# Kernel tuning notes

Measured on AMD Instinct MI355X. Metric: run time of the kernel, lower is better.

Reference implementation:

```python
import jax, jax.numpy as jnp
import numpy as np

B, T, D, H = 2, 2048, 1024, 16
HD = D // H  # head_dim = 64

def setup_inputs() -> dict:
    key = jax.random.key(0)
    ks = jax.random.split(key, 5)
    s = 0.02
    return {
        "x": jax.random.normal(ks[0], (B, T, D), dtype=jnp.float32),
        "w_qkv": jax.random.normal(ks[1], (3 * D, D), dtype=jnp.float32) * s,
        "b_qkv": jax.random.normal(ks[2], (3 * D,), dtype=jnp.float32) * s,
        "w_proj": jax.random.normal(ks[3], (D, D), dtype=jnp.float32) * s,
        "b_proj": jax.random.normal(ks[4], (D,), dtype=jnp.float32) * s,
    }

def reference(x, w_qkv, b_qkv, w_proj, b_proj):
    b, t, c = x.shape
    h, hd = H, HD
    scale = hd ** -0.5
    # qkv projection (torch Linear: x @ W^T + b)
    qkv = x @ w_qkv.T + b_qkv                      # [b, t, 3c]
    q, k, v = jnp.split(qkv, 3, axis=-1)
    # b t (h d) -> b h t d
    reshape = lambda z: z.reshape(b, t, h, hd).transpose(0, 2, 1, 3)
    q, k, v = reshape(q), reshape(k), reshape(v)
    scores = jnp.einsum("bhqd,bhkd->bhqk", q, k) * scale  # [b, h, t, t]
    causal = jnp.triu(jnp.ones((t, t), dtype=bool), k=1)   # True above diag
    scores = jnp.where(causal[None, None], -jnp.inf, scores)
    attn = jax.nn.softmax(scores, axis=-1)
    out = jnp.einsum("bhqk,bhkd->bhqd", attn, v)            # [b, h, t, d]
    out = out.transpose(0, 2, 1, 3).reshape(b, t, c)        # b h t d -> b t (h d)
    return out @ w_proj.T + b_proj
```

## Files before the change

### kernel.cpp

```cpp
#include <hip/hip_runtime.h>
#include <hip/hip_bf16.h>

#define Bq 2
#define Tq 2048
#define Dq 1024
#define Hq 16
#define HDq 64

typedef __attribute__((ext_vector_type(8))) short short8;
typedef __attribute__((ext_vector_type(4))) float f32x4;

__device__ __forceinline__ unsigned short f2bf(float f) {
  union { float f; unsigned int i; } v; v.f = f;
  unsigned int r = v.i + 0x7fffu + ((v.i >> 16) & 1u);
  return (unsigned short)(r >> 16);
}

__device__ __forceinline__ short8 cvt8(const float* __restrict__ g) {
  const float4* gp = (const float4*)g;
  float4 x0 = gp[0], x1 = gp[1];
  short8 v;
  v[0] = (short)f2bf(x0.x); v[1] = (short)f2bf(x0.y);
  v[2] = (short)f2bf(x0.z); v[3] = (short)f2bf(x0.w);
  v[4] = (short)f2bf(x1.x); v[5] = (short)f2bf(x1.y);
  v[6] = (short)f2bf(x1.z); v[7] = (short)f2bf(x1.w);
  return v;
}

__device__ __forceinline__ void async_cp16(const void* g, void* l) {
  __builtin_amdgcn_global_load_lds(
      (const __attribute__((address_space(1))) void*)g,
      (__attribute__((address_space(3))) void*)l, 16, 0, 0);
}

__device__ __forceinline__ void permswap(unsigned &a, unsigned &b) {
  asm("v_permlane32_swap_b32 %0, %1" : "+v"(a), "+v"(b));
  asm("v_permlane16_swap_b32 %0, %1" : "+v"(a), "+v"(b));
}

constexpr int NXC = (Bq * Tq * Dq) / 8;
constexpr int NW1C = (3 * Dq * Dq) / 8;
constexpr int NW2C = (Dq * Dq) / 8;

#define QSCL 0.18033688011112042f

__global__ __launch_bounds__(256)
void cvt_all(const float* __restrict__ x, const float* __restrict__ w1,
             const float* __restrict__ w2, unsigned short* __restrict__ xo,
             unsigned short* __restrict__ w1o, unsigned short* __restrict__ w2o)
{
  int i = blockIdx.x * 256 + threadIdx.x;
  const float* src; unsigned short* dst; int j;
  if (i < NXC)              { src = x;  dst = xo;  j = i; }
  else if (i < NXC + NW1C)  { src = w1; dst = w1o; j = i - NXC; }
  else                      { src = w2; dst = w2o; j = i - NXC - NW1C; }
  *(short8*)&dst[(size_t)j * 8] = cvt8(src + (size_t)j * 8);
}

template<int EPI, int BM_, int BN_>
__global__ __launch_bounds__(256)
void gemm_bt(const unsigned short* __restrict__ Ab, const unsigned short* __restrict__ Wb,
             const float* __restrict__ bias, float* __restrict__ outp,
             int K, int N,
             unsigned short* __restrict__ qo, unsigned short* __restrict__ ko,
             unsigned short* __restrict__ vo)
{
  constexpr int WM = BM_ / 2, WN = BN_ / 2;
  constexpr int NI = WM / 16;
  constexpr int NJ = WN / 16;
  constexpr int NAI = BM_ / 32;
  constexpr int NBI = BN_ / 32;
  __shared__ unsigned short As[2 * BM_ * 32];
  __shared__ unsigned short Bs[2 * BN_ * 32];

  const int t = threadIdx.x;
  const int lane = t & 63, w = t >> 6;
  const int m0 = blockIdx.y * BM_, n0 = blockIdx.x * BN_;
  const int fr = lane & 15, qd = lane >> 4;
  const int wm = (w >> 1) * WM, wn = (w & 1) * WN;

  f32x4 acc[NI][NJ] = {};

  for (int k0 = 0; k0 < K; k0 += 64) {
    __syncthreads();
    #pragma unroll
    for (int j = 0; j < NAI; j++) {
      int G = j * 256 + t;
      int panel = G / (BM_ * 4), rowg = (G / 4) % BM_, colg = G & 3;
      async_cp16(Ab + (size_t)(m0 + rowg) * K + k0 + panel * 32 + colg * 8, &As[G * 8]);
    }
    #pragma unroll
    for (int j = 0; j < NBI; j++) {
      int G = j * 256 + t;
      int panel = G / (BN_ * 4), rowg = (G / 4) % BN_, colg = G & 3;
      async_cp16(Wb + (size_t)(n0 + rowg) * K + k0 + panel * 32 + colg * 8, &Bs[G * 8]);
    }
    __syncthreads();
    #pragma unroll
    for (int kh = 0; kh < 2; kh++) {
      short8 af[NI], bf[NJ];
      #pragma unroll
      for (int ib = 0; ib < NI; ib++)
        af[ib] = *(const short8*)&As[kh * (BM_ * 32) + (wm + ib * 16 + fr) * 32 + qd * 8];
      #pragma unroll
      for (int jb = 0; jb < NJ; jb++)
        bf[jb] = *(const short8*)&Bs[kh * (BN_ * 32) + (wn + jb * 16 + fr) * 32 + qd * 8];
      #pragma unroll
      for (int ib = 0; ib < NI; ib++)
        #pragma unroll
        for (int jb = 0; jb < NJ; jb++)
          acc[ib][jb] = __builtin_amdgcn_mfma_f32_16x16x32_bf16(af[ib], bf[jb], acc[ib][jb], 0, 0, 0);
    }
  }

  #pragma unroll
  for (int jb = 0; jb < NJ; jb++) {
    int col = n0 + wn + jb * 16 + fr;
    float bv = bias[col];
    if (EPI == 0) {
      int which = col >> 10;
      int rem = col & 1023;
      int hh = rem >> 6, dd = rem & 63;
      #pragma unroll
      for (int ib = 0; ib < NI; ib++) {
        int row4 = m0 + wm + ib * 16 + qd * 4;
        int bb = row4 >> 11, tt = row4 & (Tq - 1);
        if (which == 2) {
          unsigned lo = (unsigned)f2bf(acc[ib][jb][0] + bv)
                      | ((unsigned)f2bf(acc[ib][jb][1] + bv) << 16);
          unsigned hi = (unsigned)f2bf(acc[ib][jb][2] + bv)
                      | ((unsigned)f2bf(acc[ib][jb][3] + bv) << 16);
          uint2 pk; pk.x = lo; pk.y = hi;
          *(uint2*)&vo[((size_t)(bb * Hq + hh) * HDq + dd) * Tq + tt] = pk;
        } else {
          unsigned short* dst = (which == 0) ? qo : ko;
          float scl = (which == 0) ? QSCL : 1.0f;
          #pragma unroll
          for (int r = 0; r < 4; r++)
            dst[((size_t)(bb * Hq + hh) * Tq + tt + r) * HDq + dd] =
                f2bf((acc[ib][jb][r] + bv) * scl);
        }
      }
    } else {
      #pragma unroll
      for (int ib = 0; ib < NI; ib++)
        #pragma unroll
        for (int r = 0; r < 4; r++) {
          int row = m0 + wm + ib * 16 + qd * 4 + r;
          outp[(size_t)row * N + col] = acc[ib][jb][r] + bv;
        }
    }
  }
}


template<bool DIAG>
__device__ __forceinline__ void strip_iter(
    const unsigned short* __restrict__ Ksb, const unsigned short* __restrict__ Vtsb,
    const short8 (&aq)[2], const short8 ones,
    int fr, int qd, int off0, int off1, int thr,
    f32x4 (&oacc)[4], f32x4& lacc)
{
  short8 bk[4][2];
  #pragma unroll
  for (int nb = 0; nb < 4; nb++) {
    bk[nb][0] = *(const short8*)&Ksb[(nb * 16 + fr) * 64 + off0];
    bk[nb][1] = *(const short8*)&Ksb[(nb * 16 + fr) * 64 + off1];
  }
  f32x4 s4[4] = {};
  __builtin_amdgcn_s_setprio(1);
  #pragma unroll
  for (int nb = 0; nb < 4; nb++)
    s4[nb] = __builtin_amdgcn_mfma_f32_16x16x32_bf16(bk[nb][0], aq[0], s4[nb], 0, 0, 0);
  #pragma unroll
  for (int nb = 0; nb < 4; nb++)
    s4[nb] = __builtin_amdgcn_mfma_f32_16x16x32_bf16(bk[nb][1], aq[1], s4[nb], 0, 0, 0);
  __builtin_amdgcn_s_setprio(0);

  unsigned x[4][2];
  #pragma unroll
  for (int nb = 0; nb < 4; nb++) {
    float p[4];
    #pragma unroll
    for (int reg = 0; reg < 4; reg++) {
      p[reg] = exp2f(s4[nb][reg]);
      if (DIAG && (nb * 16 + qd * 4 + reg) > thr) p[reg] = 0.f;
    }
    asm("v_cvt_pk_bf16_f32 %0, %1, %2" : "=v"(x[nb][0]) : "v"(p[0]), "v"(p[1]));
    asm("v_cvt_pk_bf16_f32 %0, %1, %2" : "=v"(x[nb][1]) : "v"(p[2]), "v"(p[3]));
  }
  permswap(x[0][0], x[1][0]);
  permswap(x[0][1], x[1][1]);
  permswap(x[2][0], x[3][0]);
  permswap(x[2][1], x[3][1]);

  short8 ap0, ap1;
  {
    union { unsigned u[4]; short8 s; } c0, c1;
    c0.u[0] = x[0][0]; c0.u[1] = x[0][1]; c0.u[2] = x[1][0]; c0.u[3] = x[1][1];
    c1.u[0] = x[2][0]; c1.u[1] = x[2][1]; c1.u[2] = x[3][0]; c1.u[3] = x[3][1];
    ap0 = c0.s; ap1 = c1.s;
  }

  short8 bv[4][2];
  #pragma unroll
  for (int db = 0; db < 4; db++) {
    bv[db][0] = *(const short8*)&Vtsb[(db * 16 + fr) * 64 + off0];
    bv[db][1] = *(const short8*)&Vtsb[(db * 16 + fr) * 64 + off1];
  }
  __builtin_amdgcn_s_setprio(1);
  lacc = __builtin_amdgcn_mfma_f32_16x16x32_bf16(ap0, ones, lacc, 0, 0, 0);
  lacc = __builtin_amdgcn_mfma_f32_16x16x32_bf16(ap1, ones, lacc, 0, 0, 0);
  #pragma unroll
  for (int db = 0; db < 4; db++) {
    oacc[db] = __builtin_amdgcn_mfma_f32_16x16x32_bf16(ap0, bv[db][0], oacc[db], 0, 0, 0);
    oacc[db] = __builtin_amdgcn_mfma_f32_16x16x32_bf16(ap1, bv[db][1], oacc[db], 0, 0, 0);
  }
  __builtin_amdgcn_s_setprio(0);
}

__global__ __launch_bounds__(256, 4)
void attn_fwd(const unsigned short* __restrict__ qb, const unsigned short* __restrict__ kb,
              const unsigned short* __restrict__ vtb, unsigned short* __restrict__ ab)
{
  __shared__ unsigned short Ks[2][64 * 64];
  __shared__ unsigned short Vts[2][64 * 64];

  const int t = threadIdx.x, w = t >> 6, lane = t & 63;
  const int fr = lane & 15, qd = lane >> 4;

  const int L  = (int)blockIdx.x;
  const int c  = L & 7;
  const int i  = L >> 3;
  const int q4 = i >> 5, j = i & 31;
  const int bh = c + 8 * q4;
  const int s  = (q4 & 1) ? j : 31 - j;
  const int s0 = s * 64;
  const int thr = w * 16 + fr;

  short8 aq[2];
  const unsigned short* Qg = qb + ((size_t)bh * Tq + s0) * HDq;
  #pragma unroll
  for (int cc = 0; cc < 2; cc++)
    aq[cc] = *(const short8*)(Qg + (w * 16 + fr) * 64 + cc * 32 + qd * 8);

  const unsigned short* Kbh = kb + (size_t)bh * Tq * HDq;
  const unsigned short* Vbh = vtb + (size_t)bh * HDq * Tq;

  const int off0 = ((qd ^ (fr & 7)) * 8);
  const int off1 = off0 ^ 32;

  const int G0 = 2 * w * 64 + lane, G1 = G0 + 64;
  const int r0 = G0 >> 3, g0 = (G0 & 7) ^ (r0 & 7);
  const int r1 = G1 >> 3, g1 = (G1 & 7) ^ (r1 & 7);

  short8 ones;
  #pragma unroll
  for (int jj = 0; jj < 8; jj++) ones[jj] = (short)0x3F80;

  f32x4 oacc[4] = {};
  f32x4 lacc = {};

  async_cp16(Kbh + (size_t)r0 * 64 + g0 * 8, &Ks[0][G0 * 8]);
  async_cp16(Vbh + (size_t)r0 * Tq + g0 * 8, &Vts[0][G0 * 8]);
  async_cp16(Kbh + (size_t)r1 * 64 + g1 * 8, &Ks[0][G1 * 8]);
  async_cp16(Vbh + (size_t)r1 * Tq + g1 * 8, &Vts[0][G1 * 8]);

  for (int kt = 0; kt < s; kt++) {
    const int cur = kt & 1, nxt = cur ^ 1;
    __syncthreads();
    const size_t kofs = (size_t)(kt + 1) * 64;
    async_cp16(Kbh + (kofs + r0) * 64 + g0 * 8, &Ks[nxt][G0 * 8]);
    async_cp16(Vbh + (size_t)r0 * Tq + kofs + g0 * 8, &Vts[nxt][G0 * 8]);
    async_cp16(Kbh + (kofs + r1) * 64 + g1 * 8, &Ks[nxt][G1 * 8]);
    async_cp16(Vbh + (size_t)r1 * Tq + kofs + g1 * 8, &Vts[nxt][G1 * 8]);
    strip_iter<false>(Ks[cur], Vts[cur], aq, ones, fr, qd, off0, off1, thr, oacc, lacc);
  }
  __syncthreads();
  strip_iter<true>(Ks[s & 1], Vts[s & 1], aq, ones, fr, qd, off0, off1, thr, oacc, lacc);

  #pragma unroll
  for (int reg = 0; reg < 4; reg++) {
    float linv = 1.0f / lacc[reg];
    size_t rowoff = ((size_t)(bh >> 4) * Tq + s0 + w * 16 + qd * 4 + reg) * Dq
                  + (bh & 15) * HDq;
    #pragma unroll
    for (int db = 0; db < 4; db++)
      ab[rowoff + db * 16 + fr] = f2bf(oacc[db][reg] * linv);
  }
}

extern "C" void kernel_launch(void* const* d_in, const int* in_sizes, int n_in,
                              void* d_out, int out_size, void* d_ws, size_t ws_size,
                              hipStream_t stream) {
  const float* x      = (const float*)d_in[0];
  const float* w_qkv  = (const float*)d_in[1];
  const float* b_qkv  = (const float*)d_in[2];
  const float* w_proj = (const float*)d_in[3];
  const float* b_proj = (const float*)d_in[4];
  float* out = (float*)d_out;

  unsigned short* ws = (unsigned short*)d_ws;
  const size_t NE = (size_t)Bq * Hq * Tq * HDq;
  unsigned short* qb  = ws;
  unsigned short* kb  = ws + NE;
  unsigned short* vtb = ws + 2 * NE;
  unsigned short* ab  = ws + 3 * NE;
  unsigned short* xb  = ws + 4 * NE;
  unsigned short* wqb = xb + (size_t)NXC * 8;
  unsigned short* wpb = wqb + (size_t)NW1C * 8;

  dim3 blk(256);
  cvt_all<<<dim3((NXC + NW1C + NW2C) >> 8), blk, 0, stream>>>(x, w_qkv, w_proj, xb, wqb, wpb);

  dim3 g1(3 * Dq / 128, Bq * Tq / 128);
  gemm_bt<0, 128, 128><<<g1, blk, 0, stream>>>(xb, wqb, b_qkv, nullptr,
                                               Dq, 3 * Dq, qb, kb, vtb);

  dim3 g2(1024);
  attn_fwd<<<g2, blk, 0, stream>>>(qb, kb, vtb, ab);

  dim3 g3(Dq / 128, Bq * Tq / 64);
  gemm_bt<1, 64, 128><<<g3, blk, 0, stream>>>(ab, wpb, b_proj, out,
                                              Dq, Dq, nullptr, nullptr, nullptr);
}
```

Baseline: 173.9 us.

## Split long causal attention strips into two KV halves with atomic-counter merge

```diff
diff --git a/kernel.cpp b/kernel.cpp
--- a/kernel.cpp
+++ b/kernel.cpp
@@ -221,7 +221,8 @@
 
 __global__ __launch_bounds__(256, 4)
 void attn_fwd(const unsigned short* __restrict__ qb, const unsigned short* __restrict__ kb,
-              const unsigned short* __restrict__ vtb, unsigned short* __restrict__ ab)
+              const unsigned short* __restrict__ vtb, unsigned short* __restrict__ ab,
+              float* __restrict__ po, float* __restrict__ pl, int* __restrict__ cnt)
 {
   __shared__ unsigned short Ks[2][64 * 64];
   __shared__ unsigned short Vts[2][64 * 64];
@@ -232,10 +233,18 @@
   const int L  = (int)blockIdx.x;
   const int c  = L & 7;
   const int i  = L >> 3;
-  const int q4 = i >> 5, j = i & 31;
-  const int bh = c + 8 * q4;
-  const int s  = (q4 & 1) ? j : 31 - j;
-  const int s0 = s * 64;
+  const int bh = c + 8 * (i / 48);
+  const int u  = i % 48;
+  int sidx, t0, t1, part;
+  if (u < 32) {
+    sidx = 31 - (u >> 1); part = u & 1;
+    const int n = sidx + 1, h = n >> 1;
+    t0 = part ? h : 0; t1 = part ? n : h;
+  } else {
+    sidx = 47 - u; part = 0; t0 = 0; t1 = sidx + 1;
+  }
+  const bool split = (u < 32);
+  const int s0 = sidx * 64;
   const int thr = w * 16 + fr;
 
   short8 aq[2];
@@ -261,32 +270,78 @@
   f32x4 oacc[4] = {};
   f32x4 lacc = {};
 
-  async_cp16(Kbh + (size_t)r0 * 64 + g0 * 8, &Ks[0][G0 * 8]);
-  async_cp16(Vbh + (size_t)r0 * Tq + g0 * 8, &Vts[0][G0 * 8]);
-  async_cp16(Kbh + (size_t)r1 * 64 + g1 * 8, &Ks[0][G1 * 8]);
-  async_cp16(Vbh + (size_t)r1 * Tq + g1 * 8, &Vts[0][G1 * 8]);
-
-  for (int kt = 0; kt < s; kt++) {
-    const int cur = kt & 1, nxt = cur ^ 1;
+  {
+    const size_t kb0 = (size_t)t0 * 64;
+    async_cp16(Kbh + (kb0 + r0) * 64 + g0 * 8, &Ks[0][G0 * 8]);
+    async_cp16(Vbh + (size_t)r0 * Tq + kb0 + g0 * 8, &Vts[0][G0 * 8]);
+    async_cp16(Kbh + (kb0 + r1) * 64 + g1 * 8, &Ks[0][G1 * 8]);
+    async_cp16(Vbh + (size_t)r1 * Tq + kb0 + g1 * 8, &Vts[0][G1 * 8]);
+  }
+
+  for (int kt = t0; kt < t1; kt++) {
+    const int cur = (kt - t0) & 1;
     __syncthreads();
-    const size_t kofs = (size_t)(kt + 1) * 64;
-    async_cp16(Kbh + (kofs + r0) * 64 + g0 * 8, &Ks[nxt][G0 * 8]);
-    async_cp16(Vbh + (size_t)r0 * Tq + kofs + g0 * 8, &Vts[nxt][G0 * 8]);
-    async_cp16(Kbh + (kofs + r1) * 64 + g1 * 8, &Ks[nxt][G1 * 8]);
-    async_cp16(Vbh + (size_t)r1 * Tq + kofs + g1 * 8, &Vts[nxt][G1 * 8]);
-    strip_iter<false>(Ks[cur], Vts[cur], aq, ones, fr, qd, off0, off1, thr, oacc, lacc);
-  }
+    if (kt + 1 < t1) {
+      const int nxt = cur ^ 1;
+      const size_t kofs = (size_t)(kt + 1) * 64;
+      async_cp16(Kbh + (kofs + r0) * 64 + g0 * 8, &Ks[nxt][G0 * 8]);
+      async_cp16(Vbh + (size_t)r0 * Tq + kofs + g0 * 8, &Vts[nxt][G0 * 8]);
+      async_cp16(Kbh + (kofs + r1) * 64 + g1 * 8, &Ks[nxt][G1 * 8]);
+      async_cp16(Vbh + (size_t)r1 * Tq + kofs + g1 * 8, &Vts[nxt][G1 * 8]);
+    }
+    if (kt == sidx)
+      strip_iter<true >(Ks[cur], Vts[cur], aq, ones, fr, qd, off0, off1, thr, oacc, lacc);
+    else
+      strip_iter<false>(Ks[cur], Vts[cur], aq, ones, fr, qd, off0, off1, thr, oacc, lacc);
+  }
+
+  if (!split) {
+    #pragma unroll
+    for (int reg = 0; reg < 4; reg++) {
+      float linv = 1.0f / lacc[reg];
+      size_t rowoff = ((size_t)(bh >> 4) * Tq + s0 + w * 16 + qd * 4 + reg) * Dq
+                    + (bh & 15) * HDq;
+      #pragma unroll
+      for (int db = 0; db < 4; db++)
+        ab[rowoff + db * 16 + fr] = f2bf(oacc[db][reg] * linv);
+    }
+    return;
+  }
+
+  const int pairid = bh * 16 + (sidx - 16);
+  const int slot = pairid * 2 + part;
+  float* poS = po + (size_t)slot * 4096;
+  float* plS = pl + (size_t)slot * 64;
+  #pragma unroll
+  for (int reg = 0; reg < 4; reg++) {
+    const int qrow = w * 16 + qd * 4 + reg;
+    plS[qrow] = lacc[reg];
+    #pragma unroll
+    for (int db = 0; db < 4; db++)
+      poS[qrow * 64 + db * 16 + fr] = oacc[db][reg];
+  }
+  __threadfence();
   __syncthreads();
-  strip_iter<true>(Ks[s & 1], Vts[s & 1], aq, ones, fr, qd, off0, off1, thr, oacc, lacc);
-
-  #pragma unroll
-  for (int reg = 0; reg < 4; reg++) {
-    float linv = 1.0f / lacc[reg];
-    size_t rowoff = ((size_t)(bh >> 4) * Tq + s0 + w * 16 + qd * 4 + reg) * Dq
-                  + (bh & 15) * HDq;
-    #pragma unroll
-    for (int db = 0; db < 4; db++)
-      ab[rowoff + db * 16 + fr] = f2bf(oacc[db][reg] * linv);
+  int* wflag = (int*)&Ks[0][0];
+  if (t == 0) wflag[0] = atomicAdd(&cnt[pairid], 1);
+  __syncthreads();
+  if (wflag[0] == 1) {
+    __threadfence();
+    const float* poA = po + (size_t)(pairid * 2) * 4096;
+    const float* poB = poA + 4096;
+    const float* plA = pl + (size_t)(pairid * 2) * 64;
+    const float* plB = plA + 64;
+    #pragma unroll
+    for (int reg = 0; reg < 4; reg++) {
+      const int qrow = w * 16 + qd * 4 + reg;
+      float linv = 1.0f / (plA[qrow] + plB[qrow]);
+      size_t rowoff = ((size_t)(bh >> 4) * Tq + s0 + qrow) * Dq + (bh & 15) * HDq;
+      #pragma unroll
+      for (int db = 0; db < 4; db++) {
+        const int idx = qrow * 64 + db * 16 + fr;
+        ab[rowoff + db * 16 + fr] = f2bf((poA[idx] + poB[idx]) * linv);
+      }
+    }
   }
 }
 
@@ -309,6 +364,9 @@
   unsigned short* xb  = ws + 4 * NE;
   unsigned short* wqb = xb + (size_t)NXC * 8;
   unsigned short* wpb = wqb + (size_t)NW1C * 8;
+  float* po  = (float*)(wpb + (size_t)NW2C * 8);
+  float* pl  = po + (size_t)1024 * 4096;
+  int*   cnt = (int*)(pl + (size_t)1024 * 64);
 
   dim3 blk(256);
   cvt_all<<<dim3((NXC + NW1C + NW2C) >> 8), blk, 0, stream>>>(x, w_qkv, w_proj, xb, wqb, wpb);
@@ -317,8 +375,9 @@
   gemm_bt<0, 128, 128><<<g1, blk, 0, stream>>>(xb, wqb, b_qkv, nullptr,
                                                Dq, 3 * Dq, qb, kb, vtb);
 
-  dim3 g2(1024);
-  attn_fwd<<<g2, blk, 0, stream>>>(qb, kb, vtb, ab);
+  hipMemsetAsync(cnt, 0, 512 * sizeof(int), stream);
+  dim3 g2(1536);
+  attn_fwd<<<g2, blk, 0, stream>>>(qb, kb, vtb, ab, po, pl, cnt);
 
   dim3 g3(Dq / 128, Bq * Tq / 64);
   gemm_bt<1, 64, 128><<<g3, blk, 0, stream>>>(ab, wpb, b_proj, out,
```

After: 362.5 us. +108.4%, slower.

## Load attention K/V tiles directly from global memory instead of LDS

Applied to the files above, without the earlier changes.

```diff
diff --git a/kernel.cpp b/kernel.cpp
--- a/kernel.cpp
+++ b/kernel.cpp
@@ -155,18 +155,26 @@
 
 
 template<bool DIAG>
-__device__ __forceinline__ void strip_iter(
-    const unsigned short* __restrict__ Ksb, const unsigned short* __restrict__ Vtsb,
+__device__ __forceinline__ void strip_iter_g(
+    const unsigned short* __restrict__ Kt,
+    const unsigned short* __restrict__ Vt,
     const short8 (&aq)[2], const short8 ones,
-    int fr, int qd, int off0, int off1, int thr,
+    int fr, int qd, int thr,
     f32x4 (&oacc)[4], f32x4& lacc)
 {
   short8 bk[4][2];
   #pragma unroll
   for (int nb = 0; nb < 4; nb++) {
-    bk[nb][0] = *(const short8*)&Ksb[(nb * 16 + fr) * 64 + off0];
-    bk[nb][1] = *(const short8*)&Ksb[(nb * 16 + fr) * 64 + off1];
-  }
+    bk[nb][0] = *(const short8*)(Kt + (nb * 16 + fr) * 64 + qd * 8);
+    bk[nb][1] = *(const short8*)(Kt + (nb * 16 + fr) * 64 + 32 + qd * 8);
+  }
+  short8 bv[4][2];
+  #pragma unroll
+  for (int db = 0; db < 4; db++) {
+    bv[db][0] = *(const short8*)(Vt + (size_t)(db * 16 + fr) * Tq + qd * 8);
+    bv[db][1] = *(const short8*)(Vt + (size_t)(db * 16 + fr) * Tq + 32 + qd * 8);
+  }
+
   f32x4 s4[4] = {};
   __builtin_amdgcn_s_setprio(1);
   #pragma unroll
@@ -202,12 +210,6 @@
     ap0 = c0.s; ap1 = c1.s;
   }
 
-  short8 bv[4][2];
-  #pragma unroll
-  for (int db = 0; db < 4; db++) {
-    bv[db][0] = *(const short8*)&Vtsb[(db * 16 + fr) * 64 + off0];
-    bv[db][1] = *(const short8*)&Vtsb[(db * 16 + fr) * 64 + off1];
-  }
   __builtin_amdgcn_s_setprio(1);
   lacc = __builtin_amdgcn_mfma_f32_16x16x32_bf16(ap0, ones, lacc, 0, 0, 0);
   lacc = __builtin_amdgcn_mfma_f32_16x16x32_bf16(ap1, ones, lacc, 0, 0, 0);
@@ -223,9 +225,6 @@
 void attn_fwd(const unsigned short* __restrict__ qb, const unsigned short* __restrict__ kb,
               const unsigned short* __restrict__ vtb, unsigned short* __restrict__ ab)
 {
-  __shared__ unsigned short Ks[2][64 * 64];
-  __shared__ unsigned short Vts[2][64 * 64];
-
   const int t = threadIdx.x, w = t >> 6, lane = t & 63;
   const int fr = lane & 15, qd = lane >> 4;
 
@@ -247,13 +246,6 @@
   const unsigned short* Kbh = kb + (size_t)bh * Tq * HDq;
   const unsigned short* Vbh = vtb + (size_t)bh * HDq * Tq;
 
-  const int off0 = ((qd ^ (fr & 7)) * 8);
-  const int off1 = off0 ^ 32;
-
-  const int G0 = 2 * w * 64 + lane, G1 = G0 + 64;
-  const int r0 = G0 >> 3, g0 = (G0 & 7) ^ (r0 & 7);
-  const int r1 = G1 >> 3, g1 = (G1 & 7) ^ (r1 & 7);
-
   short8 ones;
   #pragma unroll
   for (int jj = 0; jj < 8; jj++) ones[jj] = (short)0x3F80;
@@ -261,23 +253,11 @@
   f32x4 oacc[4] = {};
   f32x4 lacc = {};
 
-  async_cp16(Kbh + (size_t)r0 * 64 + g0 * 8, &Ks[0][G0 * 8]);
-  async_cp16(Vbh + (size_t)r0 * Tq + g0 * 8, &Vts[0][G0 * 8]);
-  async_cp16(Kbh + (size_t)r1 * 64 + g1 * 8, &Ks[0][G1 * 8]);
-  async_cp16(Vbh + (size_t)r1 * Tq + g1 * 8, &Vts[0][G1 * 8]);
-
-  for (int kt = 0; kt < s; kt++) {
-    const int cur = kt & 1, nxt = cur ^ 1;
-    __syncthreads();
-    const size_t kofs = (size_t)(kt + 1) * 64;
-    async_cp16(Kbh + (kofs + r0) * 64 + g0 * 8, &Ks[nxt][G0 * 8]);
-    async_cp16(Vbh + (size_t)r0 * Tq + kofs + g0 * 8, &Vts[nxt][G0 * 8]);
-    async_cp16(Kbh + (kofs + r1) * 64 + g1 * 8, &Ks[nxt][G1 * 8]);
-    async_cp16(Vbh + (size_t)r1 * Tq + kofs + g1 * 8, &Vts[nxt][G1 * 8]);
-    strip_iter<false>(Ks[cur], Vts[cur], aq, ones, fr, qd, off0, off1, thr, oacc, lacc);
-  }
-  __syncthreads();
-  strip_iter<true>(Ks[s & 1], Vts[s & 1], aq, ones, fr, qd, off0, off1, thr, oacc, lacc);
+  for (int kt = 0; kt < s; kt++)
+    strip_iter_g<false>(Kbh + (size_t)kt * 64 * HDq, Vbh + kt * 64,
+                        aq, ones, fr, qd, thr, oacc, lacc);
+  strip_iter_g<true>(Kbh + (size_t)s * 64 * HDq, Vbh + s * 64,
+                     aq, ones, fr, qd, thr, oacc, lacc);
 
   #pragma unroll
   for (int reg = 0; reg < 4; reg++) {
```

After: 254.3 us. 1.46x slower.
